# Kernel tuning notes

Measured on AMD Instinct MI355X. Metric: run time of the kernel, lower is better.

The kernel has to match this reference:

```python
import jax, jax.numpy as jnp
import numpy as np

# Grid / filter configuration (matches init_kwargs)
NLAT_IN, NLON_IN = 361, 720
NLAT_OUT, NLON_OUT = 361, 720
K = 9                       # kernel_size for piecewise-linear basis, kernel_shape=[3,4]
PSCALE = NLON_IN // NLON_OUT  # longitude stride between output longitudes
NNZ = 65536
B, CIN, COUT = 2, 64, 64


def setup_inputs() -> dict:
    key = jax.random.key(0)
    k0, k1, k2, k3, k4, k5 = jax.random.split(key, 6)
    x = jax.random.normal(k0, (B, CIN, NLAT_IN, NLON_IN), dtype=jnp.float32)
    psi_ker_idx = jax.random.randint(k1, (NNZ,), 0, K)
    psi_row_idx = jax.random.randint(k2, (NNZ,), 0, NLAT_OUT)
    psi_col_idx = jax.random.randint(k3, (NNZ,), 0, NLAT_IN * NLON_IN)
    # quadrature-merged, normalized basis values are small positive numbers
    psi_vals = jax.random.uniform(k4, (NNZ,), dtype=jnp.float32) / K
    scale = (1.0 / (CIN * K)) ** 0.5
    weight = scale * jax.random.normal(k5, (COUT, CIN, K), dtype=jnp.float32)
    bias = jnp.zeros((COUT,), dtype=jnp.float32)
    return {
        "x": x,
        "psi_vals": psi_vals,
        "weight": weight,
        "bias": bias,
        "psi_ker_idx": psi_ker_idx,
        "psi_row_idx": psi_row_idx,
        "psi_col_idx": psi_col_idx,
    }


def reference(x, psi_vals, weight, bias, psi_ker_idx, psi_row_idx, psi_col_idx):
    """DISCO S2 conv: y[b,c,k,lo,p] = sum_nz psi_vals * x[b,c,lat_in, (lon_in+p*PSCALE)%NLON_IN]
    restricted to nz with ker==k, row==lo; then channel mixing with weight (COUT,CIN,K) + bias.
    Matches torch fallback which rolls x by PSCALE per output longitude and does sparse bmm."""
    b, c, nlat_in, nlon_in = x.shape
    lat_in = psi_col_idx // nlon_in          # (nnz,)
    lon_in = psi_col_idx % nlon_in           # (nnz,)
    seg = psi_ker_idx * NLAT_OUT + psi_row_idx  # (nnz,) segment id over (K, nlat_out)
    xf = x.reshape(b * c, nlat_in, nlon_in)

    def step(carry, p):
        lon = (lon_in + p * PSCALE) % nlon_in        # rolled longitude index, (nnz,)
        g = xf[:, lat_in, lon]                       # (BC, nnz) gather
        contrib = (psi_vals * g).T                   # (nnz, BC)
        yk = jax.ops.segment_sum(contrib, seg, num_segments=K * NLAT_OUT)  # (K*nlat_out, BC)
        y = yk.reshape(K, NLAT_OUT, b, c)
        o = jnp.einsum("klbc,ock->bol", y, weight)   # (B, COUT, nlat_out)
        return carry, o

    _, ys = jax.lax.scan(step, None, jnp.arange(NLON_OUT))  # (nlon_out, B, COUT, nlat_out)
    out = jnp.moveaxis(ys, 0, -1)                            # (B, COUT, nlat_out, nlon_out)
    return out + bias[None, :, None, None]
```

## Files before the change

### kernel.cpp

```cpp
#include <hip/hip_runtime.h>
#include <hip/hip_cooperative_groups.h>

typedef unsigned int uint;
typedef unsigned short ushort;
typedef unsigned char uchar;

#define NLAT 361
#define NLON 720
#define NNZT 65536
#define CIN 64
#define COUT 64
#define NK 9
#define PADL 784
#define ROWCAP 384
#define CKTOT 576
#define YPS 168
#define WTS 640
#define XROWB (16*PADL*8)
#define GRIDC 722

typedef __attribute__((ext_vector_type(8))) short short8v;
typedef __attribute__((ext_vector_type(4))) float f32x4;

__device__ __forceinline__ float bfu(uint u){ return __uint_as_float(u<<16); }
__device__ __forceinline__ float bfh(uint u){ return __uint_as_float(u & 0xffff0000u); }
__device__ __forceinline__ ushort f2bf(float f){
  uint b = __float_as_uint(f);
  return (ushort)((b + 0x7fffu + ((b>>16)&1u)) >> 16);
}
__device__ __forceinline__ uint packbf2(float f0, float f1){
  uint b0 = __float_as_uint(f0), b1 = __float_as_uint(f1);
  uint r0 = (b0 + 0x7fffu + ((b0>>16)&1u)) >> 16;
  uint r1 = ((b1 + 0x7fffu + ((b1>>16)&1u)) >> 16) << 16;
  return r0 | r1;
}

__global__ __launch_bounds__(256) void k_csr(const int* __restrict__ ker, const int* __restrict__ row,
                                             const int* __restrict__ col, const float* __restrict__ vals,
                                             int2* __restrict__ meta_g, int* __restrict__ kptr_g){
  const int lo = blockIdx.x, tid = threadIdx.x;
  __shared__ int cnt[256];
  __shared__ int2 list[ROWCAP];
  __shared__ uchar kl[ROWCAP];
  __shared__ int kc[NK];
  __shared__ int ntot;
  int c=0;
  for (int i=tid;i<NNZT;i+=256) if (row[i]==lo) c++;
  cnt[tid]=c;
  if (tid<NK) kc[tid]=0;
  __syncthreads();
  if (tid==0){ int run=0; for (int t=0;t<256;t++){ int tmp=cnt[t]; cnt[t]=run; run+=tmp; } ntot=run; }
  __syncthreads();
  int off=cnt[tid];
  for (int i=tid;i<NNZT;i+=256) if (row[i]==lo){
    if (off<ROWCAP){
      int cc=col[i]; int lat=cc/NLON, lon=cc-lat*NLON;
      uint vb=__float_as_uint(vals[i])&0xfffffc00u;
      list[off]=make_int2(lat*XROWB+lon*8, (int)(vb|(uint)lon));
      kl[off]=(uchar)ker[i];
      atomicAdd(&kc[ker[i]],1);
    }
    off++;
  }
  __syncthreads();
  int n = ntot; if (n>ROWCAP) n=ROWCAP;
  for (int i=tid;i<n;i+=256){
    uint ki = ((uint)kl[i]<<23) | ((uint)list[i].x>>3);
    int r=0;
    for (int j=0;j<n;j++){
      uint kj = ((uint)kl[j]<<23) | ((uint)list[j].x>>3);
      r += (kj<ki) || (kj==ki && j<i);
    }
    meta_g[lo*ROWCAP+r]=list[i];
  }
  if (tid==0){
    int run=0;
    for (int k=0;k<NK;k++){ kptr_g[lo*10+k]=run; run+=kc[k]; }
    kptr_g[lo*10+9]=n;
  }
}

__global__ __launch_bounds__(256) void k_xb(const float* __restrict__ x, ushort* __restrict__ xb){
  const int bid=blockIdx.x, tid=threadIdx.x;
  const int b=bid/NLAT, lat=bid-b*NLAT;
  const float* xs = x + (size_t)b*CIN*NLAT*NLON + (size_t)lat*NLON;
  ushort* xd = xb + (size_t)(b*NLAT+lat)*16*PADL*4;
  const size_t S=(size_t)NLAT*NLON;
  for (int idx=tid; idx<16*PADL; idx+=256){
    int cq=idx/PADL, j=idx-cq*PADL;
    int jj = (j<NLON)? j : j-NLON;
    const float* xc = xs + (size_t)(cq*4)*S + jj;
    uint lo32 = packbf2(xc[0], xc[S]);
    uint hi32 = packbf2(xc[2*S], xc[3*S]);
    *(uint2*)(xd + (size_t)(cq*PADL + j)*4) = make_uint2(lo32, hi32);
  }
}

__global__ __launch_bounds__(256) void k_wt(const float* __restrict__ w, ushort* __restrict__ wt){
  int idx = blockIdx.x*256 + threadIdx.x;
  if (idx >= COUT*WTS) return;
  int oc = idx/WTS, ckl = idx-oc*WTS;
  int chunk = ckl/160, q = ckl-chunk*160;
  ushort v = 0;
  if (q < 144){
    int wvq=q/36, r=q-wvq*36;
    int kk=r>>2, j=r&3;
    v = f2bf(w[oc*CKTOT + (chunk*16 + wvq*4 + j)*NK + kk]);
  }
  wt[oc*WTS + ckl] = v;
}

template<int USE_XB, int SYNC>
__global__ __launch_bounds__(256,4) void k_coop(const float* __restrict__ x, const ushort* __restrict__ xb,
    const int2* __restrict__ meta_g, const int* __restrict__ kptr_g,
    const ushort* __restrict__ wt, const float* __restrict__ bias, float* __restrict__ out){
  const int wid=blockIdx.x, tid=threadIdx.x;
  const int lane=tid&63, wv=tid>>6, l15=lane&15, kg=lane>>4;
  const int lo=wid>>1, b=wid&1;

  __shared__ int2 meta[ROWCAP];
  __shared__ __align__(16) ushort Yp[64*YPS];

  int kp[10];
  #pragma unroll
  for (int kk=0;kk<10;kk++){ int v=kptr_g[lo*10+kk]; kp[kk]=v<ROWCAP?v:ROWCAP; }
  for (int i=tid;i<kp[9];i+=256) meta[i]=meta_g[lo*ROWCAP+i];
  for (int idx=tid; idx<64*8; idx+=256){
    int p=idx>>3, j=idx&7;
    *(uint*)((char*)Yp + p*(YPS*2) + 288 + j*4)=0;
  }
  __syncthreads();

  const int wvu = __builtin_amdgcn_readfirstlane(wv);
  const char* xb8 = (const char*)xb + (size_t)b*NLAT*(size_t)XROWB;
  const char* wtb = (const char*)wt + ((wv*16+l15)*WTS + kg*8)*2;
  const char* ypb = (const char*)Yp + l15*(YPS*2) + kg*16;
  char* ydst = (char*)Yp + lane*(YPS*2) + wv*72;

#define GADDR(M) ((uint)(M).x + lanep8 + (((((uint)(M).y)&0x3ffu) >= thr) ? (uint)-5760 : 0u))
#define GVAL(M)  __uint_as_float(((uint)(M).y) & 0xfffffc00u)
#define GCONS(U,V,ACC,AI) { ACC[0][AI]+=(V)*bfu((U).x); ACC[1][AI]+=(V)*bfh((U).x); \
                            ACC[2][AI]+=(V)*bfu((U).y); ACC[3][AI]+=(V)*bfh((U).y); }
#define GB1F(M,ACC,AI) { \
      uint lon=((uint)(M).y)&0x3ffu; float v=GVAL(M); \
      int lat=(int)(((uint)(M).x)/(uint)XROWB); \
      int s=(int)lon+p0; s=(s>=NLON)?s-NLON:s; \
      int widx=s+lane; widx=(widx>=NLON)?widx-NLON:widx; \
      int fb=((b*CIN + chunk*16 + wv*4)*NLAT + lat)*NLON + widx; \
      ACC[0][AI]+=v*x[fb]; ACC[1][AI]+=v*x[fb+NLAT*NLON]; \
      ACC[2][AI]+=v*x[fb+2*NLAT*NLON]; ACC[3][AI]+=v*x[fb+3*NLAT*NLON]; }

#define GSEG(ACC,KI,AI) { \
      int i=kp[KI]; const int e=kp[(KI)+1]; \
      if (USE_XB){ \
        for (; i+7<e; i+=8){ \
          int2 m0=meta[i],m1=meta[i+1],m2=meta[i+2],m3=meta[i+3]; \
          int2 m4=meta[i+4],m5=meta[i+5],m6=meta[i+6],m7=meta[i+7]; \
          uint2 u0=*(const uint2*)(xbase+GADDR(m0)); uint2 u1=*(const uint2*)(xbase+GADDR(m1)); \
          uint2 u2=*(const uint2*)(xbase+GADDR(m2)); uint2 u3=*(const uint2*)(xbase+GADDR(m3)); \
          uint2 u4=*(const uint2*)(xbase+GADDR(m4)); uint2 u5=*(const uint2*)(xbase+GADDR(m5)); \
          uint2 u6=*(const uint2*)(xbase+GADDR(m6)); uint2 u7=*(const uint2*)(xbase+GADDR(m7)); \
          GCONS(u0,GVAL(m0),ACC,AI); GCONS(u1,GVAL(m1),ACC,AI); \
          GCONS(u2,GVAL(m2),ACC,AI); GCONS(u3,GVAL(m3),ACC,AI); \
          GCONS(u4,GVAL(m4),ACC,AI); GCONS(u5,GVAL(m5),ACC,AI); \
          GCONS(u6,GVAL(m6),ACC,AI); GCONS(u7,GVAL(m7),ACC,AI); \
        } \
        for (; i+3<e; i+=4){ \
          int2 m0=meta[i],m1=meta[i+1],m2=meta[i+2],m3=meta[i+3]; \
          uint2 u0=*(const uint2*)(xbase+GADDR(m0)); uint2 u1=*(const uint2*)(xbase+GADDR(m1)); \
          uint2 u2=*(const uint2*)(xbase+GADDR(m2)); uint2 u3=*(const uint2*)(xbase+GADDR(m3)); \
          GCONS(u0,GVAL(m0),ACC,AI); GCONS(u1,GVAL(m1),ACC,AI); \
          GCONS(u2,GVAL(m2),ACC,AI); GCONS(u3,GVAL(m3),ACC,AI); \
        } \
        for (; i<e; i++){ int2 m0=meta[i]; \
          uint2 u0=*(const uint2*)(xbase+GADDR(m0)); GCONS(u0,GVAL(m0),ACC,AI); } \
      } else { \
        for (; i<e; i++){ int2 m0=meta[i]; GB1F(m0,ACC,AI); } \
      } }

  f32x4 outacc[3][4];
  #pragma unroll
  for (int a=0;a<3;a++)
    #pragma unroll
    for (int c2=0;c2<4;c2++) outacc[a][c2]=(f32x4)0.f;

  for (int pt=0;pt<4;pt++){
    for (int chunk=0;chunk<4;chunk++){
      if constexpr (SYNC) cooperative_groups::this_grid().sync();
      const char* xbase = xb8 + (size_t)(chunk*4+wvu)*(PADL*8);
      for (int it=0;it<3;it++){
        const int p0 = it*240 + pt*64;
        const uint thr = (uint)(NLON-p0);
        const uint lanep8 = (uint)(lane+p0)*8u;
        const bool act = (pt<3) || (lane<48);

        {
          float acc1[4][5];
          #pragma unroll
          for (int j=0;j<4;j++)
            #pragma unroll
            for (int kk=0;kk<5;kk++) acc1[j][kk]=0.f;
          if (act){ GSEG(acc1,0,0) GSEG(acc1,1,1) GSEG(acc1,2,2) GSEG(acc1,3,3) GSEG(acc1,4,4) }
          __syncthreads();
          if (act){
            #pragma unroll
            for (int kk=0;kk<5;kk++){
              *(uint*)(ydst + (kk*4+0)*2) = packbf2(acc1[0][kk], acc1[1][kk]);
              *(uint*)(ydst + (kk*4+2)*2) = packbf2(acc1[2][kk], acc1[3][kk]);
            }
          }
        }
        {
          float acc2[4][4];
          #pragma unroll
          for (int j=0;j<4;j++)
            #pragma unroll
            for (int kk=0;kk<4;kk++) acc2[j][kk]=0.f;
          if (act){
            GSEG(acc2,5,0) GSEG(acc2,6,1) GSEG(acc2,7,2) GSEG(acc2,8,3)
            #pragma unroll
            for (int kk=0;kk<4;kk++){
              *(uint*)(ydst + ((kk+5)*4+0)*2) = packbf2(acc2[0][kk], acc2[1][kk]);
              *(uint*)(ydst + ((kk+5)*4+2)*2) = packbf2(acc2[2][kk], acc2[3][kk]);
            }
          }
        }
        __syncthreads();
        #pragma unroll
        for (int ptile=0;ptile<4;ptile++){
          #pragma unroll
          for (int ks=0;ks<5;ks++){
            short8v bf = *(const short8v*)(ypb + ptile*(16*YPS*2) + ks*64);
            short8v afk = *(const short8v*)(wtb + (chunk*160 + ks*32)*2);
            outacc[it][ptile]=__builtin_amdgcn_mfma_f32_16x16x32_bf16(afk,bf,outacc[it][ptile],0,0,0);
          }
        }
      }
    }
    #pragma unroll
    for (int it=0;it<3;it++){
      #pragma unroll
      for (int ptile=0;ptile<4;ptile++){
        const int pidx = pt*64 + ptile*16;
        if (pidx < 240){
          #pragma unroll
          for (int r=0;r<4;r++){
            int oc = wv*16 + kg*4 + r;
            out[((size_t)(b*COUT+oc)*NLAT + lo)*NLON + it*240 + pidx + l15]
              = outacc[it][ptile][r] + bias[oc];
          }
        }
        outacc[it][ptile]=(f32x4)0.f;
      }
    }
  }
#undef GSEG
#undef GB1F
#undef GCONS
#undef GVAL
#undef GADDR
}

extern "C" void kernel_launch(void* const* d_in, const int* in_sizes, int n_in,
                              void* d_out, int out_size, void* d_ws, size_t ws_size,
                              hipStream_t stream){
  const float* x   =(const float*)d_in[0];
  const float* vals=(const float*)d_in[1];
  const float* w   =(const float*)d_in[2];
  const float* bias=(const float*)d_in[3];
  const int* ker=(const int*)d_in[4];
  const int* row=(const int*)d_in[5];
  const int* col=(const int*)d_in[6];
  float* outp=(float*)d_out;

  const size_t META_B=(size_t)NLAT*ROWCAP*sizeof(int2);
  const size_t KPTR_B=((size_t)NLAT*10*sizeof(int)+15)&~(size_t)15;
  const size_t WT_B=((size_t)COUT*WTS*sizeof(ushort)+15)&~(size_t)15;
  const size_t XB_B=(size_t)2*NLAT*16*PADL*4*sizeof(ushort);
  int2* meta_g=(int2*)d_ws;
  int*  kptr_g=(int*)((char*)d_ws+META_B);
  ushort* wt=(ushort*)((char*)d_ws+META_B+KPTR_B);
  ushort* xb=(ushort*)((char*)d_ws+META_B+KPTR_B+WT_B);
  const bool use_xb = ws_size >= META_B+KPTR_B+WT_B+XB_B;

  k_csr<<<dim3(NLAT), dim3(256), 0, stream>>>(ker,row,col,vals,meta_g,kptr_g);
  k_wt <<<dim3((COUT*WTS+255)/256), dim3(256), 0, stream>>>(w, wt);
  if (use_xb)
    k_xb<<<dim3(2*NLAT), dim3(256), 0, stream>>>(x, xb);

  int dev=0; (void)hipGetDevice(&dev);
  int coopAttr=0; (void)hipDeviceGetAttribute(&coopAttr, hipDeviceAttributeCooperativeLaunch, dev);
  int ncu=0; (void)hipDeviceGetAttribute(&ncu, hipDeviceAttributeMultiprocessorCount, dev);

  typedef void (*KFn)(const float*, const ushort*, const int2*, const int*,
                      const ushort*, const float*, float*);
  KFn fsync = use_xb ? (KFn)&k_coop<1,1> : (KFn)&k_coop<0,1>;
  int nb=0;
  (void)hipOccupancyMaxActiveBlocksPerMultiprocessor(&nb, fsync, 256, 0);

  bool coop = (coopAttr!=0) && ((long)nb*(long)ncu >= (long)GRIDC);
  if (coop){
    const ushort* xbc = xb; const ushort* wtc = wt;
    const int2* mgc = meta_g; const int* kpc = kptr_g;
    void* params[7] = {(void*)&x,(void*)&xbc,(void*)&mgc,(void*)&kpc,(void*)&wtc,(void*)&bias,(void*)&outp};
    hipError_t e = hipLaunchCooperativeKernel(reinterpret_cast<const void*>(fsync),
                                              dim3(GRIDC), dim3(256), params, 0, stream);
    if (e != hipSuccess){ (void)hipGetLastError(); coop=false; }
  }
  if (!coop){
    if (use_xb) k_coop<1,0><<<dim3(GRIDC), dim3(256), 0, stream>>>(x,xb,meta_g,kptr_g,wt,bias,outp);
    else        k_coop<0,0><<<dim3(GRIDC), dim3(256), 0, stream>>>(x,xb,meta_g,kptr_g,wt,bias,outp);
  }
}
```

Before: 2.063 ms.

## Band-sort nonzeros by address before kernel index and halve grid syncs

The CSR build now ranks each row's nonzeros by gather address and splits them into six address bands. Within each band they are sorted by kernel index, and per-(band, kernel) offsets are stored. The main kernel walks the bands in order and sums each kernel segment inside a band, so successive gathers for all kernel indices hit nearby x rows. The aim is better cache reuse than sweeping the whole address range once per kernel index. It also issues the cooperative grid sync only every other chunk, cutting sync overhead but loosening the lockstep between blocks. The cost is shorter segments, which run more remainder loops and do less 8-way unrolling, plus a heavier preprocessing sort.

```diff
diff --git a/kernel.cpp b/kernel.cpp
--- a/kernel.cpp
+++ b/kernel.cpp
@@ -18,6 +18,8 @@
 #define WTS 640
 #define XROWB (16*PADL*8)
 #define GRIDC 722
+#define NB 6
+#define KPSTRIDE 56
 
 typedef __attribute__((ext_vector_type(8))) short short8v;
 typedef __attribute__((ext_vector_type(4))) float f32x4;
@@ -42,12 +44,13 @@
   __shared__ int cnt[256];
   __shared__ int2 list[ROWCAP];
   __shared__ uchar kl[ROWCAP];
-  __shared__ int kc[NK];
+  __shared__ ushort r0s[ROWCAP];
+  __shared__ int cntbk[NB*9];
   __shared__ int ntot;
   int c=0;
   for (int i=tid;i<NNZT;i+=256) if (row[i]==lo) c++;
   cnt[tid]=c;
-  if (tid<NK) kc[tid]=0;
+  if (tid<NB*9) cntbk[tid]=0;
   __syncthreads();
   if (tid==0){ int run=0; for (int t=0;t<256;t++){ int tmp=cnt[t]; cnt[t]=run; run+=tmp; } ntot=run; }
   __syncthreads();
@@ -58,25 +61,40 @@
       uint vb=__float_as_uint(vals[i])&0xfffffc00u;
       list[off]=make_int2(lat*XROWB+lon*8, (int)(vb|(uint)lon));
       kl[off]=(uchar)ker[i];
-      atomicAdd(&kc[ker[i]],1);
     }
     off++;
   }
   __syncthreads();
   int n = ntot; if (n>ROWCAP) n=ROWCAP;
   for (int i=tid;i<n;i+=256){
-    uint ki = ((uint)kl[i]<<23) | ((uint)list[i].x>>3);
+    uint xi=(uint)list[i].x; int r=0;
+    for (int j=0;j<n;j++){
+      uint xj=(uint)list[j].x;
+      r += (xj<xi) || (xj==xi && j<i);
+    }
+    r0s[i]=(ushort)r;
+  }
+  __syncthreads();
+  for (int i=tid;i<n;i+=256){
+    int band=((int)r0s[i]*NB)/n;
+    atomicAdd(&cntbk[band*9+(int)kl[i]],1);
+  }
+  __syncthreads();
+  if (tid==0){
+    int run=0;
+    for (int j=0;j<NB*9;j++){ kptr_g[lo*KPSTRIDE+j]=run; run+=cntbk[j]; }
+    kptr_g[lo*KPSTRIDE+NB*9]=n;
+  }
+  for (int i=tid;i<n;i+=256){
+    uint bi=((uint)r0s[i]*(uint)NB)/(uint)n;
+    uint keyi=(bi<<27)|((uint)kl[i]<<23)|((uint)list[i].x>>3);
     int r=0;
     for (int j=0;j<n;j++){
-      uint kj = ((uint)kl[j]<<23) | ((uint)list[j].x>>3);
-      r += (kj<ki) || (kj==ki && j<i);
+      uint bj=((uint)r0s[j]*(uint)NB)/(uint)n;
+      uint keyj=(bj<<27)|((uint)kl[j]<<23)|((uint)list[j].x>>3);
+      r += (keyj<keyi) || (keyj==keyi && j<i);
     }
     meta_g[lo*ROWCAP+r]=list[i];
-  }
-  if (tid==0){
-    int run=0;
-    for (int k=0;k<NK;k++){ kptr_g[lo*10+k]=run; run+=kc[k]; }
-    kptr_g[lo*10+9]=n;
   }
 }
 
@@ -120,11 +138,11 @@
 
   __shared__ int2 meta[ROWCAP];
   __shared__ __align__(16) ushort Yp[64*YPS];
-
-  int kp[10];
-  #pragma unroll
-  for (int kk=0;kk<10;kk++){ int v=kptr_g[lo*10+kk]; kp[kk]=v<ROWCAP?v:ROWCAP; }
-  for (int i=tid;i<kp[9];i+=256) meta[i]=meta_g[lo*ROWCAP+i];
+  __shared__ int Sl[NB*9+1];
+
+  int n = kptr_g[lo*KPSTRIDE+NB*9]; if (n>ROWCAP) n=ROWCAP;
+  for (int i=tid;i<NB*9+1;i+=256) Sl[i]=kptr_g[lo*KPSTRIDE+i];
+  for (int i=tid;i<n;i+=256) meta[i]=meta_g[lo*ROWCAP+i];
   for (int idx=tid; idx<64*8; idx+=256){
     int p=idx>>3, j=idx&7;
     *(uint*)((char*)Yp + p*(YPS*2) + 288 + j*4)=0;
@@ -150,8 +168,8 @@
       ACC[0][AI]+=v*x[fb]; ACC[1][AI]+=v*x[fb+NLAT*NLON]; \
       ACC[2][AI]+=v*x[fb+2*NLAT*NLON]; ACC[3][AI]+=v*x[fb+3*NLAT*NLON]; }
 
-#define GSEG(ACC,KI,AI) { \
-      int i=kp[KI]; const int e=kp[(KI)+1]; \
+#define GSEG(ACC,B0,E0,AI) { \
+      int i=(B0); const int e=(E0); \
       if (USE_XB){ \
         for (; i+7<e; i+=8){ \
           int2 m0=meta[i],m1=meta[i+1],m2=meta[i+2],m3=meta[i+3]; \
@@ -186,12 +204,12 @@
 
   for (int pt=0;pt<4;pt++){
     for (int chunk=0;chunk<4;chunk++){
-      if constexpr (SYNC) cooperative_groups::this_grid().sync();
+      if constexpr (SYNC){ if ((chunk&1)==0) cooperative_groups::this_grid().sync(); }
       const char* xbase = xb8 + (size_t)(chunk*4+wvu)*(PADL*8);
       for (int it=0;it<3;it++){
         const int p0 = it*240 + pt*64;
         const uint thr = (uint)(NLON-p0);
-        const uint lanep8 = (uint)(lane+p0)*8u;
+        const uint lanep8 = (uint)(lane + p0)*8u;
         const bool act = (pt<3) || (lane<48);
 
         {
@@ -200,7 +218,16 @@
           for (int j=0;j<4;j++)
             #pragma unroll
             for (int kk=0;kk<5;kk++) acc1[j][kk]=0.f;
-          if (act){ GSEG(acc1,0,0) GSEG(acc1,1,1) GSEG(acc1,2,2) GSEG(acc1,3,3) GSEG(acc1,4,4) }
+          if (act){
+            for (int b6=0;b6<NB;b6++){
+              int kpB[6];
+              #pragma unroll
+              for (int j=0;j<6;j++) kpB[j]=Sl[b6*9+j];
+              GSEG(acc1,kpB[0],kpB[1],0) GSEG(acc1,kpB[1],kpB[2],1)
+              GSEG(acc1,kpB[2],kpB[3],2) GSEG(acc1,kpB[3],kpB[4],3)
+              GSEG(acc1,kpB[4],kpB[5],4)
+            }
+          }
           __syncthreads();
           if (act){
             #pragma unroll
@@ -217,7 +244,13 @@
             #pragma unroll
             for (int kk=0;kk<4;kk++) acc2[j][kk]=0.f;
           if (act){
-            GSEG(acc2,5,0) GSEG(acc2,6,1) GSEG(acc2,7,2) GSEG(acc2,8,3)
+            for (int b6=0;b6<NB;b6++){
+              int kpB[5];
+              #pragma unroll
+              for (int j=0;j<5;j++) kpB[j]=Sl[b6*9+5+j];
+              GSEG(acc2,kpB[0],kpB[1],0) GSEG(acc2,kpB[1],kpB[2],1)
+              GSEG(acc2,kpB[2],kpB[3],2) GSEG(acc2,kpB[3],kpB[4],3)
+            }
             #pragma unroll
             for (int kk=0;kk<4;kk++){
               *(uint*)(ydst + ((kk+5)*4+0)*2) = packbf2(acc2[0][kk], acc2[1][kk]);
@@ -274,7 +307,7 @@
   float* outp=(float*)d_out;
 
   const size_t META_B=(size_t)NLAT*ROWCAP*sizeof(int2);
-  const size_t KPTR_B=((size_t)NLAT*10*sizeof(int)+15)&~(size_t)15;
+  const size_t KPTR_B=((size_t)NLAT*KPSTRIDE*sizeof(int)+15)&~(size_t)15;
   const size_t WT_B=((size_t)COUT*WTS*sizeof(ushort)+15)&~(size_t)15;
   const size_t XB_B=(size_t)2*NLAT*16*PADL*4*sizeof(ushort);
   int2* meta_g=(int2*)d_ws;
```

Result: slower. 2.827 ms (+37.0%).
